# Kernel tuning notes

Hardware: AMD Instinct MI355X
Metric: run time of the kernel (lower is better)

The kernel has to match this reference:

```python
import jax, jax.numpy as jnp
import numpy as np

SIGMA = 0.2


def setup_inputs() -> dict:
    key = jax.random.key(0)
    k1, k2, k3, k4 = jax.random.split(key, 4)
    n = 50000
    normal = jax.random.normal(k1, (n, 3), dtype=jnp.float32)
    neighbour = jax.random.randint(k2, (n, 3), 0, n, dtype=jnp.int64)
    theta_par = jax.random.uniform(k3, (1, 64, 4), dtype=jnp.float32) * np.pi
    phi_par = jax.random.uniform(k4, (1, 64, 4), dtype=jnp.float32) * (2 * np.pi)
    return {"normal": normal, "neighbour": neighbour,
            "theta_par": theta_par, "phi_par": phi_par}


def reference(normal, neighbour, theta_par, phi_par):
    # kernel points on the unit sphere: [3, 64, 4] (coords, M kernels, L points)
    kernel = jnp.concatenate(
        [jnp.sin(theta_par) * jnp.sin(phi_par),
         jnp.sin(theta_par) * jnp.cos(phi_par),
         jnp.cos(theta_par)], axis=0)
    # gather self + 3 neighbour normals: pts [n, 4, 3]
    neigh = normal[neighbour]                      # [n, 3, 3]
    pts = jnp.concatenate([normal[:, None, :], neigh], axis=1)  # [n, 4, 3]
    # squared distance between each point and each kernel point,
    # summed over coords: [n, 4(points), 64, 4(kernel pts)]
    diff = pts[:, :, :, None, None] - kernel[None, None, :, :, :]
    correl = jnp.sum(diff * diff, axis=2)          # [n, 4, 64, 4]
    resp = jnp.exp(correl / (-2.0 * SIGMA * SIGMA))
    fea = jnp.sum(resp, axis=(1, 3)) / 16.0        # [n, 64]
    return fea
```

## Files before the change

kernel.cpp:

```cpp
#include <hip/hip_runtime.h>
#include <math.h>

#define SIGMA 0.2f
#define LOG2E 1.4426950408889634f

__global__ __launch_bounds__(1024) void corr_kernel(
    const float* __restrict__ normal,
    const int*   __restrict__ neighbour,
    const float* __restrict__ theta,
    const float* __restrict__ phi,
    float*       __restrict__ out,
    int n)
{
    __shared__ float kx[256], ky[256], kz[256];
    const int t = threadIdx.x;

    if (t < 256) {
        const int km = t >> 2;
        const int kl = t & 3;
        float th = theta[t];
        float ph = phi[t];
        float st = __sinf(th), ct = __cosf(th);
        float sp = __sinf(ph), cp = __cosf(ph);
        const float s = LOG2E / (SIGMA * SIGMA);
        kx[kl * 64 + km] = st * sp * s;
        ky[kl * 64 + km] = st * cp * s;
        kz[kl * 64 + km] = ct * s;
    }
    __syncthreads();

    const int m = t & 63;
    const int w = t >> 6;
    const int i = blockIdx.x * 16 + w;
    if (i >= n) return;

    const int id1 = neighbour[i * 3 + 0];
    const int id2 = neighbour[i * 3 + 1];
    const int id3 = neighbour[i * 3 + 2];

    float px[4], py[4], pz[4];
    px[0] = normal[(long long)i * 3 + 0];
    py[0] = normal[(long long)i * 3 + 1];
    pz[0] = normal[(long long)i * 3 + 2];
    px[1] = normal[(long long)id1 * 3 + 0];
    py[1] = normal[(long long)id1 * 3 + 1];
    pz[1] = normal[(long long)id1 * 3 + 2];
    px[2] = normal[(long long)id2 * 3 + 0];
    py[2] = normal[(long long)id2 * 3 + 1];
    pz[2] = normal[(long long)id2 * 3 + 2];
    px[3] = normal[(long long)id3 * 3 + 0];
    py[3] = normal[(long long)id3 * 3 + 1];
    pz[3] = normal[(long long)id3 * 3 + 2];

    float kxs[4], kys[4], kzs[4];
#pragma unroll
    for (int l = 0; l < 4; ++l) {
        kxs[l] = kx[l * 64 + m];
        kys[l] = ky[l * 64 + m];
        kzs[l] = kz[l * 64 + m];
    }

    const float c1 = -LOG2E / (2.0f * SIGMA * SIGMA);

    float acc0 = 0.0f, acc1 = 0.0f;
#pragma unroll
    for (int p = 0; p < 4; ++p) {
        const float c2 = (px[p] * px[p] + py[p] * py[p] + pz[p] * pz[p] + 1.0f) * c1;
        acc0 += __builtin_amdgcn_exp2f(fmaf(px[p], kxs[0], fmaf(py[p], kys[0], fmaf(pz[p], kzs[0], c2))));
        acc1 += __builtin_amdgcn_exp2f(fmaf(px[p], kxs[1], fmaf(py[p], kys[1], fmaf(pz[p], kzs[1], c2))));
        acc0 += __builtin_amdgcn_exp2f(fmaf(px[p], kxs[2], fmaf(py[p], kys[2], fmaf(pz[p], kzs[2], c2))));
        acc1 += __builtin_amdgcn_exp2f(fmaf(px[p], kxs[3], fmaf(py[p], kys[3], fmaf(pz[p], kzs[3], c2))));
    }

    out[(long long)i * 64 + m] = (acc0 + acc1) * (1.0f / 16.0f);
}

extern "C" void kernel_launch(void* const* d_in, const int* in_sizes, int n_in,
                              void* d_out, int out_size, void* d_ws, size_t ws_size,
                              hipStream_t stream) {
    const float* normal    = (const float*)d_in[0];
    const int*   neighbour = (const int*)d_in[1];
    const float* theta     = (const float*)d_in[2];
    const float* phi       = (const float*)d_in[3];
    float*       out       = (float*)d_out;

    const int n = in_sizes[0] / 3;
    const int blocks = (n + 15) / 16;

    hipLaunchKernelGGL(corr_kernel, dim3(blocks), dim3(1024), 0, stream,
                       normal, neighbour, theta, phi, out, n);
}
```

Measured before the change: 22.08 us.

## Precompute kernel-point table in separate launch and shrink blocks to 256 threads

Moves the per-block sin/cos computation of the kernel points into a one-block setup kernel that writes a float4 table to workspace. The main kernel now loads the table from global memory (cache-resident) instead of recomputing it in every block with shared memory and a barrier. Blocks shrink from 1024 to 256 threads, the accumulators are split four ways, and indexing uses 32-bit arithmetic. The cost is an extra kernel launch and a dependency between the two launches.

After: 25.61 us. +16.0%, slower.

```diff
diff --git a/kernel.cpp b/kernel.cpp
--- a/kernel.cpp
+++ b/kernel.cpp
@@ -4,75 +4,71 @@
 #define SIGMA 0.2f
 #define LOG2E 1.4426950408889634f
 
-__global__ __launch_bounds__(1024) void corr_kernel(
-    const float* __restrict__ normal,
-    const int*   __restrict__ neighbour,
+__global__ __launch_bounds__(256) void corr_setup(
     const float* __restrict__ theta,
     const float* __restrict__ phi,
-    float*       __restrict__ out,
+    float4*      __restrict__ table)
+{
+    const int t = threadIdx.x;
+    const int m = t >> 2;
+    const int l = t & 3;
+    const float th = theta[t];
+    const float ph = phi[t];
+    const float st = sinf(th), ct = cosf(th);
+    const float sp = sinf(ph), cp = cosf(ph);
+    const float s = LOG2E / (SIGMA * SIGMA);
+    table[l * 64 + m] = make_float4(st * sp * s, st * cp * s, ct * s, 0.0f);
+}
+
+__global__ __launch_bounds__(256) void corr_main(
+    const float*  __restrict__ normal,
+    const int*    __restrict__ neighbour,
+    const float4* __restrict__ table,
+    float*        __restrict__ out,
     int n)
 {
-    __shared__ float kx[256], ky[256], kz[256];
     const int t = threadIdx.x;
-
-    if (t < 256) {
-        const int km = t >> 2;
-        const int kl = t & 3;
-        float th = theta[t];
-        float ph = phi[t];
-        float st = __sinf(th), ct = __cosf(th);
-        float sp = __sinf(ph), cp = __cosf(ph);
-        const float s = LOG2E / (SIGMA * SIGMA);
-        kx[kl * 64 + km] = st * sp * s;
-        ky[kl * 64 + km] = st * cp * s;
-        kz[kl * 64 + km] = ct * s;
-    }
-    __syncthreads();
-
     const int m = t & 63;
     const int w = t >> 6;
-    const int i = blockIdx.x * 16 + w;
+    const int i = blockIdx.x * 4 + w;
     if (i >= n) return;
+
+    const float4 k0 = table[  0 + m];
+    const float4 k1 = table[ 64 + m];
+    const float4 k2 = table[128 + m];
+    const float4 k3 = table[192 + m];
 
     const int id1 = neighbour[i * 3 + 0];
     const int id2 = neighbour[i * 3 + 1];
     const int id3 = neighbour[i * 3 + 2];
 
     float px[4], py[4], pz[4];
-    px[0] = normal[(long long)i * 3 + 0];
-    py[0] = normal[(long long)i * 3 + 1];
-    pz[0] = normal[(long long)i * 3 + 2];
-    px[1] = normal[(long long)id1 * 3 + 0];
-    py[1] = normal[(long long)id1 * 3 + 1];
-    pz[1] = normal[(long long)id1 * 3 + 2];
-    px[2] = normal[(long long)id2 * 3 + 0];
-    py[2] = normal[(long long)id2 * 3 + 1];
-    pz[2] = normal[(long long)id2 * 3 + 2];
-    px[3] = normal[(long long)id3 * 3 + 0];
-    py[3] = normal[(long long)id3 * 3 + 1];
-    pz[3] = normal[(long long)id3 * 3 + 2];
-
-    float kxs[4], kys[4], kzs[4];
-#pragma unroll
-    for (int l = 0; l < 4; ++l) {
-        kxs[l] = kx[l * 64 + m];
-        kys[l] = ky[l * 64 + m];
-        kzs[l] = kz[l * 64 + m];
-    }
+    px[0] = normal[i * 3 + 0];
+    py[0] = normal[i * 3 + 1];
+    pz[0] = normal[i * 3 + 2];
+    px[1] = normal[id1 * 3 + 0];
+    py[1] = normal[id1 * 3 + 1];
+    pz[1] = normal[id1 * 3 + 2];
+    px[2] = normal[id2 * 3 + 0];
+    py[2] = normal[id2 * 3 + 1];
+    pz[2] = normal[id2 * 3 + 2];
+    px[3] = normal[id3 * 3 + 0];
+    py[3] = normal[id3 * 3 + 1];
+    pz[3] = normal[id3 * 3 + 2];
 
     const float c1 = -LOG2E / (2.0f * SIGMA * SIGMA);
 
-    float acc0 = 0.0f, acc1 = 0.0f;
+    float acc0 = 0.0f, acc1 = 0.0f, acc2 = 0.0f, acc3 = 0.0f;
 #pragma unroll
     for (int p = 0; p < 4; ++p) {
-        const float c2 = (px[p] * px[p] + py[p] * py[p] + pz[p] * pz[p] + 1.0f) * c1;
-        acc0 += __builtin_amdgcn_exp2f(fmaf(px[p], kxs[0], fmaf(py[p], kys[0], fmaf(pz[p], kzs[0], c2))));
-        acc1 += __builtin_amdgcn_exp2f(fmaf(px[p], kxs[1], fmaf(py[p], kys[1], fmaf(pz[p], kzs[1], c2))));
-        acc0 += __builtin_amdgcn_exp2f(fmaf(px[p], kxs[2], fmaf(py[p], kys[2], fmaf(pz[p], kzs[2], c2))));
-        acc1 += __builtin_amdgcn_exp2f(fmaf(px[p], kxs[3], fmaf(py[p], kys[3], fmaf(pz[p], kzs[3], c2))));
+        const float c2 = fmaf(px[p], px[p], fmaf(py[p], py[p], fmaf(pz[p], pz[p], 1.0f))) * c1;
+        acc0 += __builtin_amdgcn_exp2f(fmaf(px[p], k0.x, fmaf(py[p], k0.y, fmaf(pz[p], k0.z, c2))));
+        acc1 += __builtin_amdgcn_exp2f(fmaf(px[p], k1.x, fmaf(py[p], k1.y, fmaf(pz[p], k1.z, c2))));
+        acc2 += __builtin_amdgcn_exp2f(fmaf(px[p], k2.x, fmaf(py[p], k2.y, fmaf(pz[p], k2.z, c2))));
+        acc3 += __builtin_amdgcn_exp2f(fmaf(px[p], k3.x, fmaf(py[p], k3.y, fmaf(pz[p], k3.z, c2))));
     }
 
-    out[(long long)i * 64 + m] = (acc0 + acc1) * (1.0f / 16.0f);
+    out[i * 64 + m] = ((acc0 + acc1) + (acc2 + acc3)) * (1.0f / 16.0f);
 }
 
 extern "C" void kernel_launch(void* const* d_in, const int* in_sizes, int n_in,
@@ -83,10 +79,14 @@
     const float* theta     = (const float*)d_in[2];
     const float* phi       = (const float*)d_in[3];
     float*       out       = (float*)d_out;
+    float4*      table     = (float4*)d_ws;
 
     const int n = in_sizes[0] / 3;
-    const int blocks = (n + 15) / 16;
 
-    hipLaunchKernelGGL(corr_kernel, dim3(blocks), dim3(1024), 0, stream,
-                       normal, neighbour, theta, phi, out, n);
+    hipLaunchKernelGGL(corr_setup, dim3(1), dim3(256), 0, stream,
+                       theta, phi, table);
+
+    const int blocks = (n + 3) / 4;
+    hipLaunchKernelGGL(corr_main, dim3(blocks), dim3(256), 0, stream,
+                       normal, neighbour, table, out, n);
 }
```
